# Performance work log

Measured on AMD Instinct MI355X. Metric: run time of the kernel, lower is better.

## Reference

```python
import jax, jax.numpy as jnp
import numpy as np

B, H, W = 64, 512, 512
HW = H * W
MIN_, MAX_ = 100, 100          # seeds sampled per image (bg, fg)
MIN_P, MAX_P = 0.3, 0.3        # candidate-pool fractions
FG_ERODE_K, FG_ERODE_ITER = 11, 1
KSZ = 3                        # dilation kernel for seed maps
IGNORE_IDX = -255
N_BG = int(MIN_P * H * W)      # static bottom-n pool size
EPS = 1e-8


def _minpool2d(x, k):  # morphological erosion of binary map (geodesic border)
    return jax.lax.reduce_window(x, np.inf, jax.lax.min, (k, k), (1, 1), 'SAME')


def _maxpool3d(x, k):  # morphological dilation over (b,h,w)
    return jax.lax.reduce_window(x, -np.inf, jax.lax.max, (1, k, k), (1, 1, 1), 'SAME')


def _gumbel(u):
    return -jnp.log(-jnp.log(u))


def _one_sample(cam, u_fg, u_bg, th):
    # cam: [H,W] in [0,1]; u_fg/u_bg: [HW] uniform(0,1); th: scalar threshold
    cam_q = jnp.floor(cam * 255.0)
    th = jnp.where(th == 0.0, 1.0, jnp.where(th == 255.0, 254.0, th))
    deg = cam.min() == cam.max()  # degenerate map -> no seeds
    roi = (cam_q > th).astype(jnp.float32)
    for _ in range(FG_ERODE_ITER):
        roi = _minpool2d(roi, FG_ERODE_K)

    # ---- foreground: top-n of cam*roi, weighted sample max_ w/o replacement
    camr = (cam * roi + EPS).reshape(HW)
    n_fg = jnp.floor(MAX_P * roi.sum()).astype(jnp.int32)
    order = jnp.argsort(-camr, stable=True)                 # descending stable
    rank = jnp.zeros(HW, jnp.int32).at[order].set(jnp.arange(HW, dtype=jnp.int32))
    mask = rank < n_fg
    logp = jnp.log(jnp.where(mask, camr, 1.0))              # weighted: p = cam value
    score = jnp.where(mask, logp + _gumbel(u_fg), -jnp.inf) # Gumbel top-k == multinomial w/o repl.
    _, sel = jax.lax.top_k(score, MAX_)
    valid = (jnp.arange(MAX_) < jnp.minimum(MAX_, n_fg)) & (n_fg > 0) & (~deg)
    fg = jnp.zeros(HW, jnp.int32).at[sel].set(valid.astype(jnp.int32))

    # ---- background: bottom-n of cam, weighted by relu(1-cam)+eps
    camb = (cam + EPS).reshape(HW)
    orderb = jnp.argsort(camb, stable=True)                 # ascending stable
    rankb = jnp.zeros(HW, jnp.int32).at[orderb].set(jnp.arange(HW, dtype=jnp.int32))
    maskb = rankb < N_BG
    pb = jax.nn.relu(1.0 - camb) + EPS
    scoreb = jnp.where(maskb, jnp.log(pb) + _gumbel(u_bg), -jnp.inf)
    _, selb = jax.lax.top_k(scoreb, MIN_)
    validb = (jnp.arange(MIN_) < min(MIN_, N_BG)) & (~deg)
    bg = jnp.zeros(HW, jnp.int32).at[selb].set(validb.astype(jnp.int32))

    return fg.reshape(H, W), bg.reshape(H, W)


def setup_inputs() -> dict:
    key = jax.random.key(0)
    k1, k2, k3, k4 = jax.random.split(key, 4)
    x = jax.random.uniform(k1, (B, 1, H, W), dtype=jnp.float32)
    roi_thresh = jax.random.randint(k2, (B,), 0, 200).astype(jnp.float32)
    u_fg = jax.random.uniform(k3, (B, HW), dtype=jnp.float32, minval=1e-6, maxval=1.0)
    u_bg = jax.random.uniform(k4, (B, HW), dtype=jnp.float32, minval=1e-6, maxval=1.0)
    return {"x": x, "roi_thresh": roi_thresh, "u_fg": u_fg, "u_bg": u_bg}


def reference(x, roi_thresh, u_fg, u_bg):
    cam = x[:, 0]  # [B,H,W]
    all_fg, all_bg = jax.vmap(_one_sample)(cam, u_fg, u_bg, roi_thresh)
    if KSZ > 1:
        all_fg = (_maxpool3d(all_fg.astype(jnp.float32), KSZ) > 0.5).astype(jnp.int32)
        all_bg = (_maxpool3d(all_bg.astype(jnp.float32), KSZ) > 0.5).astype(jnp.int32)
    outer = all_fg + all_bg
    all_fg = jnp.where(outer == 2, 0, all_fg)
    all_bg = jnp.where(outer == 2, 0, all_bg)
    out = jnp.full((B, H, W), IGNORE_IDX, dtype=jnp.int32)
    out = jnp.where(all_fg == 1, 1, out)
    out = jnp.where(all_bg == 1, 0, out)
    return out
```

## Files before the change

### kernel.cpp

```cpp
#include <hip/hip_runtime.h>

typedef unsigned int u32;

#define BB 64
#define HH 512
#define WW 512
#define HWP 262144
#define WPI 8192
#define NBV 1024
#define NBS 512
#define EPSF 1e-8f
#define NBGK 78643
#define CAND_CAP 4096
#define SEL_CAP 128
#define PN 12
#define CP 16


__device__ __forceinline__ int vbucket(float vb){
    int b = (int)(vb * (float)NBV);
    b = b < 0 ? 0 : b;
    return b > (NBV-1) ? (NBV-1) : b;
}
__device__ __forceinline__ int sbucket(float s){
    float a = (s + 24.0f) * ((float)NBS / 44.0f);
    a = fmaxf(a, 0.0f);
    int b = (int)a;
    return b > (NBS-1) ? (NBS-1) : b;
}
__device__ __forceinline__ u32 flipf(float s){
    u32 u = __float_as_uint(s);
    u32 m = (u & 0x80000000u) ? 0xFFFFFFFFu : 0x80000000u;
    return u ^ m;
}

template<int NB, int BPT, bool DESC>
__device__ __forceinline__ void hist_kth(const u32* __restrict__ hh, int target,
        int* partial, int* res, int t){
    int s = 0;
    #pragma unroll
    for (int i = 0; i < BPT; i++){
        int b = DESC ? (NB-1 - (t*BPT+i)) : (t*BPT+i);
        s += (int)hh[b];
    }
    partial[t] = s;
    __syncthreads();
    for (int off = 1; off < 256; off <<= 1){
        int v = partial[t];
        int u = (t >= off) ? partial[t-off] : 0;
        __syncthreads();
        partial[t] = v + u;
        __syncthreads();
    }
    int incl = partial[t];
    int above = incl - s;
    if (above < target && target <= incl){
        int cum = above;
        #pragma unroll
        for (int i = 0; i < BPT; i++){
            int b = DESC ? (NB-1 - (t*BPT+i)) : (t*BPT+i);
            int h = (int)hh[b];
            if (cum + h >= target){ res[0] = b; res[1] = target - cum; break; }
            cum += h;
        }
    }
    __syncthreads();
}

__global__ __launch_bounds__(256) void k_prep(const float* __restrict__ x,
        const float* __restrict__ thr, u32* __restrict__ roiH,
        u32* __restrict__ ghist_bg, u32* __restrict__ minb, u32* __restrict__ maxb)
{
    __shared__ u32 hist[NBV];
    __shared__ u32 A[256];
    int t = threadIdx.x;
    for (int i = t; i < NBV; i += 256) hist[i] = 0u;
    A[t] = 0u;
    __syncthreads();
    int img = blockIdx.x >> 5, blk = blockIdx.x & 31;
    const float4* c4 = (const float4*)x + (size_t)img * (HWP/4) + (size_t)blk * 2048;
    float th = thr[img];
    th = (th == 0.0f) ? 1.0f : ((th == 255.0f) ? 254.0f : th);
    float4 v[8];
    #pragma unroll
    for (int k = 0; k < 8; k++) v[k] = c4[k*256 + t];
    u32 mn = 0xFFFFFFFFu, mx = 0u;
    #pragma unroll
    for (int k = 0; k < 8; k++){
        float vv[4] = {v[k].x, v[k].y, v[k].z, v[k].w};
        u32 nib = 0u;
        #pragma unroll
        for (int c = 0; c < 4; c++){
            float vl = vv[c];
            u32 ub = __float_as_uint(vl);
            mn = mn < ub ? mn : ub;
            mx = mx > ub ? mx : ub;
            if (floorf(vl * 255.0f) > th) nib |= (1u << c);
            atomicAdd(&hist[vbucket(vl + EPSF)], 1u);
        }
        if (nib) atomicOr(&A[k*32 + (t>>3)], nib << ((t&7)*4));
    }
    for (int o = 32; o >= 1; o >>= 1){
        u32 m2 = __shfl_down(mn, o); mn = mn < m2 ? mn : m2;
        u32 m3 = __shfl_down(mx, o); mx = mx > m3 ? mx : m3;
    }
    if ((t & 63) == 0){ atomicMin(&minb[img], mn); atomicMax(&maxb[img], mx); }
    __syncthreads();
    {
        int wr = t & 15;
        u32 cur = A[t];
        u32 left  = (wr > 0)  ? A[t-1] : 0xFFFFFFFFu;
        u32 right = (wr < 15) ? A[t+1] : 0xFFFFFFFFu;
        u32 res = cur;
        #pragma unroll
        for (int d = 1; d <= 5; d++){
            res &= (cur >> d) | (right << (32 - d));
            res &= (cur << d) | (left  >> (32 - d));
        }
        roiH[(size_t)img*WPI + blk*256 + t] = res;
    }
    for (int i = t; i < NBV; i += 256){
        u32 h = hist[i];
        if (h) atomicAdd(&ghist_bg[(size_t)img*NBV + i], h);
    }
}

__global__ __launch_bounds__(256) void k_vfg(const float* __restrict__ x,
        const u32* __restrict__ roiH, u32* __restrict__ roiE,
        u32* __restrict__ roiSum, u32* __restrict__ ghist_fg)
{
    __shared__ u32 hist[NBV];
    __shared__ u32 W[256];
    int t = threadIdx.x;
    for (int i = t; i < NBV; i += 256) hist[i] = 0u;
    int img = blockIdx.x >> 5, blk = blockIdx.x & 31;
    const u32* rp = roiH + (size_t)img * WPI;
    int iw = blk*256 + t;
    int r = iw >> 4;
    u32 res = 0xFFFFFFFFu;
    #pragma unroll
    for (int d = -5; d <= 5; d++){
        int rr = r + d;
        if (rr >= 0 && rr < HH) res &= rp[iw + d*16];
    }
    W[t] = res;
    roiE[(size_t)img*WPI + iw] = res;
    u32 cnt = __popc(res);
    for (int o = 32; o >= 1; o >>= 1) cnt += __shfl_down(cnt, o);
    if ((t & 63) == 0) atomicAdd(&roiSum[img], cnt);
    __syncthreads();
    const float4* c4 = (const float4*)x + (size_t)img * (HWP/4) + (size_t)blk * 2048;
    u32 nb[8];
    float4 vv[8];
    #pragma unroll
    for (int k = 0; k < 8; k++){
        nb[k] = (W[k*32 + (t>>3)] >> ((t&7)*4)) & 0xFu;
        if (nb[k]) vv[k] = c4[k*256 + t];
    }
    #pragma unroll
    for (int k = 0; k < 8; k++){
        if (nb[k]){
            float vl[4] = {vv[k].x, vv[k].y, vv[k].z, vv[k].w};
            #pragma unroll
            for (int c = 0; c < 4; c++){
                if ((nb[k] >> c) & 1u) atomicAdd(&hist[vbucket(vl[c] + EPSF)], 1u);
            }
        }
    }
    __syncthreads();
    for (int i = t; i < NBV; i += 256){
        u32 h = hist[i];
        if (h) atomicAdd(&ghist_fg[(size_t)img*NBV + i], h);
    }
}

__global__ __launch_bounds__(256) void k_collect1(const float* __restrict__ x, const u32* __restrict__ roiE,
        const u32* __restrict__ ghf, const u32* __restrict__ ghb,
        const u32* __restrict__ minb, const u32* __restrict__ maxb, const u32* __restrict__ roiSum,
        int* __restrict__ prm,
        uint2* __restrict__ candF, u32* __restrict__ cntF,
        uint2* __restrict__ candB, u32* __restrict__ cntB)
{
    __shared__ int partial[256];
    __shared__ int res[2];
    __shared__ u32 words[256];
    int img = blockIdx.x >> 5, blk = blockIdx.x & 31, t = threadIdx.x;
    int deg = (minb[img] == maxb[img]) ? 1 : 0;
    int nfg = (int)floorf(0.3f * (float)(int)roiSum[img]);
    int Bf = -1, rf = 0, Bb = -1, rb = 0;
    if (!deg && nfg > 0){
        hist_kth<NBV,4,true>(ghf + (size_t)img*NBV, nfg, partial, res, t);
        Bf = res[0]; rf = res[1];
    }
    if (!deg){
        hist_kth<NBV,4,false>(ghb + (size_t)img*NBV, NBGK, partial, res, t);
        Bb = res[0]; rb = res[1];
    }
    if (blk == 0 && t == 0){
        int* p = prm + img*PN;
        p[0] = nfg; p[1] = deg; p[2] = Bf; p[3] = rf; p[4] = Bb; p[5] = rb;
    }
    words[t] = roiE[(size_t)img*WPI + blk*256 + t];
    __syncthreads();
    const float4* c4 = (const float4*)x + (size_t)img * (HWP/4) + (size_t)blk * 2048;
    float4 v[8];
    #pragma unroll
    for (int k = 0; k < 8; k++) v[k] = c4[k*256 + t];
    #pragma unroll
    for (int k = 0; k < 8; k++){
        float vv[4] = {v[k].x, v[k].y, v[k].z, v[k].w};
        u32 nib = (words[k*32 + (t>>3)] >> ((t&7)*4)) & 0xFu;
        int pix0 = blk*8192 + k*1024 + t*4;
        #pragma unroll
        for (int c = 0; c < 4; c++){
            float vb = vv[c] + EPSF;
            int bkt = vbucket(vb);
            int pix = pix0 + c;
            if (bkt == Bb){
                u32 q = atomicAdd(&cntB[img*CP], 1u);
                if (q < CAND_CAP) candB[(size_t)img*CAND_CAP + q] = make_uint2(__float_as_uint(vb), (u32)pix);
            }
            if (bkt == Bf && ((nib >> c) & 1u)){
                u32 q = atomicAdd(&cntF[img*CP], 1u);
                if (q < CAND_CAP) candF[(size_t)img*CAND_CAP + q] = make_uint2(__float_as_uint(vb), (u32)pix);
            }
        }
    }
}

__global__ __launch_bounds__(256) void k_resolve1(const uint2* __restrict__ candF, const u32* __restrict__ cntF,
        const uint2* __restrict__ candB, const u32* __restrict__ cntB, int* __restrict__ prm)
{
    int b = blockIdx.x, t = threadIdx.x;
    __shared__ uint2 c[CAND_CAP];
    int rf = prm[b*PN + 3];
    if (rf > 0){
        int m = (int)cntF[b*CP]; m = m < CAND_CAP ? m : CAND_CAP;
        for (int i = t; i < m; i += 256) c[i] = candF[(size_t)b*CAND_CAP + i];
        __syncthreads();
        for (int i = t; i < m; i += 256){
            u32 ki = c[i].x, xi = c[i].y;
            int r = 0;
            for (int j = 0; j < m; j++){
                u32 kj = c[j].x, xj = c[j].y;
                r += (kj > ki) || (kj == ki && xj < xi);
            }
            if (r == rf - 1){ prm[b*PN + 6] = (int)ki; prm[b*PN + 7] = (int)xi; }
        }
    } else if (t == 0){
        prm[b*PN + 6] = (int)0xFFFFFFFFu; prm[b*PN + 7] = -1;
    }
    __syncthreads();
    int rb = prm[b*PN + 5];
    if (rb > 0){
        int m = (int)cntB[b*CP]; m = m < CAND_CAP ? m : CAND_CAP;
        for (int i = t; i < m; i += 256) c[i] = candB[(size_t)b*CAND_CAP + i];
        __syncthreads();
        for (int i = t; i < m; i += 256){
            u32 ki = c[i].x, xi = c[i].y;
            int r = 0;
            for (int j = 0; j < m; j++){
                u32 kj = c[j].x, xj = c[j].y;
                r += (kj < ki) || (kj == ki && xj < xi);
            }
            if (r == rb - 1){ prm[b*PN + 8] = (int)ki; prm[b*PN + 9] = (int)xi; }
        }
    } else if (t == 0){
        prm[b*PN + 8] = 0; prm[b*PN + 9] = -1;
    }
}

__global__ __launch_bounds__(256) void k_shist(const float* __restrict__ x, const u32* __restrict__ roiE,
        const float* __restrict__ ufg, const float* __restrict__ ubg, const int* __restrict__ prm,
        u32* __restrict__ shfG, u32* __restrict__ shbG)
{
    __shared__ u32 hf[NBS];
    __shared__ u32 hb[NBS];
    __shared__ u32 words[256];
    int t = threadIdx.x;
    for (int i = t; i < NBS; i += 256){ hf[i] = 0u; hb[i] = 0u; }
    int img = blockIdx.x >> 5, blk = blockIdx.x & 31;
    words[t] = roiE[(size_t)img*WPI + blk*256 + t];
    __syncthreads();
    const int* p = prm + img*PN;
    u32 ubf = (u32)p[6]; int ibf = p[7];
    u32 ubb = (u32)p[8]; int ibb = p[9];
    size_t b4 = (size_t)img * (HWP/4) + (size_t)blk * 2048;
    const float4* c4 = (const float4*)x + b4;
    const float4* uf4 = (const float4*)ufg + b4;
    const float4* ub4 = (const float4*)ubg + b4;
    float4 v[8];
    #pragma unroll
    for (int k = 0; k < 8; k++) v[k] = c4[k*256 + t];
    u32 fmsk = 0u, bmsk = 0u;
    #pragma unroll
    for (int k = 0; k < 8; k++){
        float vv[4] = {v[k].x, v[k].y, v[k].z, v[k].w};
        u32 nib = (words[k*32 + (t>>3)] >> ((t&7)*4)) & 0xFu;
        int pix0 = blk*8192 + k*1024 + t*4;
        #pragma unroll
        for (int c = 0; c < 4; c++){
            float vb = vv[c] + EPSF;
            u32 bu = __float_as_uint(vb);
            int pix = pix0 + c;
            if (((nib >> c) & 1u) && (bu > ubf || (bu == ubf && pix <= ibf))) fmsk |= 1u << (k*4+c);
            if (bu < ubb || (bu == ubb && pix <= ibb)) bmsk |= 1u << (k*4+c);
        }
    }
    float4 uf[8];
    #pragma unroll
    for (int k = 0; k < 8; k++) if ((fmsk >> (k*4)) & 0xFu) uf[k] = uf4[k*256 + t];
    #pragma unroll
    for (int k = 0; k < 8; k++){
        if ((fmsk >> (k*4)) & 0xFu){
            float vv[4] = {v[k].x, v[k].y, v[k].z, v[k].w};
            float uu[4] = {uf[k].x, uf[k].y, uf[k].z, uf[k].w};
            #pragma unroll
            for (int c = 0; c < 4; c++){
                if ((fmsk >> (k*4+c)) & 1u){
                    float s = logf(vv[c] + EPSF) - logf(-logf(uu[c]));
                    atomicAdd(&hf[sbucket(s)], 1u);
                }
            }
        }
    }
    float4 ub[8];
    #pragma unroll
    for (int k = 0; k < 8; k++) if ((bmsk >> (k*4)) & 0xFu) ub[k] = ub4[k*256 + t];
    #pragma unroll
    for (int k = 0; k < 8; k++){
        if ((bmsk >> (k*4)) & 0xFu){
            float vv[4] = {v[k].x, v[k].y, v[k].z, v[k].w};
            float uu[4] = {ub[k].x, ub[k].y, ub[k].z, ub[k].w};
            #pragma unroll
            for (int c = 0; c < 4; c++){
                if ((bmsk >> (k*4+c)) & 1u){
                    float pb = fmaxf(1.0f - (vv[c] + EPSF), 0.0f) + EPSF;
                    float s = logf(pb) - logf(-logf(uu[c]));
                    atomicAdd(&hb[sbucket(s)], 1u);
                }
            }
        }
    }
    __syncthreads();
    for (int i = t; i < NBS; i += 256){
        u32 h = hf[i]; if (h) atomicAdd(&shfG[(size_t)img*NBS + i], h);
        h = hb[i];     if (h) atomicAdd(&shbG[(size_t)img*NBS + i], h);
    }
}

__global__ __launch_bounds__(256) void k_collect2(const float* __restrict__ x, const u32* __restrict__ roiE,
        const float* __restrict__ ufg, const float* __restrict__ ubg, const int* __restrict__ prm,
        const u32* __restrict__ shfG, const u32* __restrict__ shbG,
        uint2* __restrict__ selF, u32* __restrict__ cntSelF, uint2* __restrict__ scandF, u32* __restrict__ cntScF,
        uint2* __restrict__ selB, u32* __restrict__ cntSelB, uint2* __restrict__ scandB, u32* __restrict__ cntScB)
{
    __shared__ int partial[256];
    __shared__ int res[2];
    __shared__ u32 words[256];
    int img = blockIdx.x >> 5, blk = blockIdx.x & 31, t = threadIdx.x;
    const int* p = prm + img*PN;
    int nfg = p[0], deg = p[1];
    int kf = (deg || nfg <= 0) ? 0 : (nfg < 100 ? nfg : 100);
    int kb = deg ? 0 : 100;
    int sbf = 0x7FFFFFFF, sbb = 0x7FFFFFFF;
    if (kf > 0){
        hist_kth<NBS,2,true>(shfG + (size_t)img*NBS, kf, partial, res, t);
        sbf = res[0];
    }
    if (kb > 0){
        hist_kth<NBS,2,true>(shbG + (size_t)img*NBS, kb, partial, res, t);
        sbb = res[0];
    }
    u32 ubf = (u32)p[6]; int ibf = p[7];
    u32 ubb = (u32)p[8]; int ibb = p[9];
    words[t] = roiE[(size_t)img*WPI + blk*256 + t];
    __syncthreads();
    size_t b4 = (size_t)img * (HWP/4) + (size_t)blk * 2048;
    const float4* c4 = (const float4*)x + b4;
    const float4* uf4 = (const float4*)ufg + b4;
    const float4* ub4 = (const float4*)ubg + b4;
    float4 v[8];
    #pragma unroll
    for (int k = 0; k < 8; k++) v[k] = c4[k*256 + t];
    u32 fmsk = 0u, bmsk = 0u;
    #pragma unroll
    for (int k = 0; k < 8; k++){
        float vv[4] = {v[k].x, v[k].y, v[k].z, v[k].w};
        u32 nib = (words[k*32 + (t>>3)] >> ((t&7)*4)) & 0xFu;
        int pix0 = blk*8192 + k*1024 + t*4;
        #pragma unroll
        for (int c = 0; c < 4; c++){
            float vb = vv[c] + EPSF;
            u32 bu = __float_as_uint(vb);
            int pix = pix0 + c;
            if (((nib >> c) & 1u) && (bu > ubf || (bu == ubf && pix <= ibf))) fmsk |= 1u << (k*4+c);
            if (bu < ubb || (bu == ubb && pix <= ibb)) bmsk |= 1u << (k*4+c);
        }
    }
    float4 uf[8];
    #pragma unroll
    for (int k = 0; k < 8; k++) if ((fmsk >> (k*4)) & 0xFu) uf[k] = uf4[k*256 + t];
    #pragma unroll
    for (int k = 0; k < 8; k++){
        if ((fmsk >> (k*4)) & 0xFu){
            float vv[4] = {v[k].x, v[k].y, v[k].z, v[k].w};
            float uu[4] = {uf[k].x, uf[k].y, uf[k].z, uf[k].w};
            int pix0 = blk*8192 + k*1024 + t*4;
            #pragma unroll
            for (int c = 0; c < 4; c++){
                if ((fmsk >> (k*4+c)) & 1u){
                    float s = logf(vv[c] + EPSF) - logf(-logf(uu[c]));
                    int sb = sbucket(s);
                    if (sb > sbf){
                        u32 q = atomicAdd(&cntSelF[img*CP], 1u);
                        if (q < SEL_CAP) selF[(size_t)img*SEL_CAP + q] = make_uint2(flipf(s), (u32)(pix0 + c));
                    } else if (sb == sbf){
                        u32 q = atomicAdd(&cntScF[img*CP], 1u);
                        if (q < CAND_CAP) scandF[(size_t)img*CAND_CAP + q] = make_uint2(flipf(s), (u32)(pix0 + c));
                    }
                }
            }
        }
    }
    float4 ub[8];
    #pragma unroll
    for (int k = 0; k < 8; k++) if ((bmsk >> (k*4)) & 0xFu) ub[k] = ub4[k*256 + t];
    #pragma unroll
    for (int k = 0; k < 8; k++){
        if ((bmsk >> (k*4)) & 0xFu){
            float vv[4] = {v[k].x, v[k].y, v[k].z, v[k].w};
            float uu[4] = {ub[k].x, ub[k].y, ub[k].z, ub[k].w};
            int pix0 = blk*8192 + k*1024 + t*4;
            #pragma unroll
            for (int c = 0; c < 4; c++){
                if ((bmsk >> (k*4+c)) & 1u){
                    float pb = fmaxf(1.0f - (vv[c] + EPSF), 0.0f) + EPSF;
                    float s = logf(pb) - logf(-logf(uu[c]));
                    int sb = sbucket(s);
                    if (sb > sbb){
                        u32 q = atomicAdd(&cntSelB[img*CP], 1u);
                        if (q < SEL_CAP) selB[(size_t)img*SEL_CAP + q] = make_uint2(flipf(s), (u32)(pix0 + c));
                    } else if (sb == sbb){
                        u32 q = atomicAdd(&cntScB[img*CP], 1u);
                        if (q < CAND_CAP) scandB[(size_t)img*CAND_CAP + q] = make_uint2(flipf(s), (u32)(pix0 + c));
                    }
                }
            }
        }
    }
}

__global__ __launch_bounds__(256) void k_seeds(
        const uint2* __restrict__ selF, const u32* __restrict__ cntSelF,
        const uint2* __restrict__ scandF, const u32* __restrict__ cntScF,
        const uint2* __restrict__ selB, const u32* __restrict__ cntSelB,
        const uint2* __restrict__ scandB, const u32* __restrict__ cntScB,
        const u32* __restrict__ shfG, const u32* __restrict__ shbG,
        const int* __restrict__ prm,
        int* __restrict__ gSeedF, int* __restrict__ gnF,
        int* __restrict__ gSeedB, int* __restrict__ gnB)
{
    int b = blockIdx.x, t = threadIdx.x;
    __shared__ uint2 c[CAND_CAP];
    __shared__ int partial[256];
    __shared__ int res[2];
    __shared__ int seedF[SEL_CAP];
    __shared__ int seedB[SEL_CAP];
    __shared__ int nF, nB;
    const int* p = prm + b*PN;
    int nfg = p[0], deg = p[1];
    int kf = (deg || nfg <= 0) ? 0 : (nfg < 100 ? nfg : 100);
    int kb = deg ? 0 : 100;
    int needf = 0, needb = 0;
    if (kf > 0){
        hist_kth<NBS,2,true>(shfG + (size_t)b*NBS, kf, partial, res, t);
        needf = res[1];
    }
    if (kb > 0){
        hist_kth<NBS,2,true>(shbG + (size_t)b*NBS, kb, partial, res, t);
        needb = res[1];
    }

    int c0 = (int)cntSelF[b*CP]; c0 = c0 < SEL_CAP ? c0 : SEL_CAP;
    for (int i = t; i < c0; i += 256) seedF[i] = (int)selF[(size_t)b*SEL_CAP + i].y;
    int m = (int)cntScF[b*CP]; m = m < CAND_CAP ? m : CAND_CAP;
    for (int i = t; i < m; i += 256) c[i] = scandF[(size_t)b*CAND_CAP + i];
    if (t == 0){ nF = c0; nB = 0; }
    __syncthreads();
    for (int i = t; i < m; i += 256){
        u32 ki = c[i].x, xi = c[i].y;
        int r = 0;
        for (int j = 0; j < m; j++){
            u32 kj = c[j].x, xj = c[j].y;
            r += (kj > ki) || (kj == ki && xj < xi);
        }
        if (r < needf){
            int q = atomicAdd(&nF, 1);
            if (q < SEL_CAP) seedF[q] = (int)xi;
        }
    }
    __syncthreads();
    int fN = nF; fN = fN < SEL_CAP ? fN : SEL_CAP;
    __syncthreads();

    int c0b = (int)cntSelB[b*CP]; c0b = c0b < SEL_CAP ? c0b : SEL_CAP;
    for (int i = t; i < c0b; i += 256) seedB[i] = (int)selB[(size_t)b*SEL_CAP + i].y;
    int mb = (int)cntScB[b*CP]; mb = mb < CAND_CAP ? mb : CAND_CAP;
    for (int i = t; i < mb; i += 256) c[i] = scandB[(size_t)b*CAND_CAP + i];
    if (t == 0) nB = c0b;
    __syncthreads();
    for (int i = t; i < mb; i += 256){
        u32 ki = c[i].x, xi = c[i].y;
        int r = 0;
        for (int j = 0; j < mb; j++){
            u32 kj = c[j].x, xj = c[j].y;
            r += (kj > ki) || (kj == ki && xj < xi);
        }
        if (r < needb){
            int q = atomicAdd(&nB, 1);
            if (q < SEL_CAP) seedB[q] = (int)xi;
        }
    }
    __syncthreads();
    int bN = nB; bN = bN < SEL_CAP ? bN : SEL_CAP;

    for (int i = t; i < fN; i += 256) gSeedF[b*SEL_CAP + i] = seedF[i];
    for (int i = t; i < bN; i += 256) gSeedB[b*SEL_CAP + i] = seedB[i];
    if (t == 0){ gnF[b] = fN; gnB[b] = bN; }
}

__global__ __launch_bounds__(256) void k_paint(
        const int* __restrict__ gSeedF, const int* __restrict__ gnF,
        const int* __restrict__ gSeedB, const int* __restrict__ gnB,
        int* __restrict__ out)
{
    __shared__ int sF[SEL_CAP], sB[SEL_CAP];
    int img = blockIdx.x >> 5, blk = blockIdx.x & 31, t = threadIdx.x;
    int fN = gnF[img]; fN = fN < SEL_CAP ? fN : SEL_CAP;
    int bN = gnB[img]; bN = bN < SEL_CAP ? bN : SEL_CAP;
    for (int i = t; i < fN; i += 256) sF[i] = gSeedF[img*SEL_CAP + i];
    for (int i = t; i < bN; i += 256) sB[i] = gSeedB[img*SEL_CAP + i];
    int4* o4 = (int4*)(out + (size_t)img*HWP + blk*8192);
    #pragma unroll
    for (int i = 0; i < 8; i++) o4[i*256 + t] = make_int4(-255,-255,-255,-255);
    __syncthreads();
    int row0 = blk * 16;
    int* outp = out + (size_t)img*HWP;
    for (int task = t; task < fN * 9; task += 256){
        int s = sF[task / 9];
        int o = task % 9;
        int y = (s >> 9) + (o / 3) - 1;
        int xx = (s & 511) + (o % 3) - 1;
        if (y < row0 || y >= row0 + 16 || xx < 0 || xx >= WW) continue;
        bool conf = false;
        for (int j = 0; j < bN; j++){
            int sb2 = sB[j];
            int dy = y - (sb2 >> 9); if (dy < 0) dy = -dy;
            int dx = xx - (sb2 & 511); if (dx < 0) dx = -dx;
            if (dy <= 1 && dx <= 1){ conf = true; break; }
        }
        if (!conf) outp[y * WW + xx] = 1;
    }
    for (int task = t; task < bN * 9; task += 256){
        int s = sB[task / 9];
        int o = task % 9;
        int y = (s >> 9) + (o / 3) - 1;
        int xx = (s & 511) + (o % 3) - 1;
        if (y < row0 || y >= row0 + 16 || xx < 0 || xx >= WW) continue;
        bool conf = false;
        for (int j = 0; j < fN; j++){
            int sf2 = sF[j];
            int dy = y - (sf2 >> 9); if (dy < 0) dy = -dy;
            int dx = xx - (sf2 & 511); if (dx < 0) dx = -dx;
            if (dy <= 1 && dx <= 1){ conf = true; break; }
        }
        if (!conf) outp[y * WW + xx] = 0;
    }
}

extern "C" void kernel_launch(void* const* d_in, const int* in_sizes, int n_in,
                              void* d_out, int out_size, void* d_ws, size_t ws_size,
                              hipStream_t stream)
{
    (void)in_sizes; (void)n_in; (void)out_size; (void)ws_size;
    const float* x   = (const float*)d_in[0];
    const float* thr = (const float*)d_in[1];
    const float* ufg = (const float*)d_in[2];
    const float* ubg = (const float*)d_in[3];
    int* out = (int*)d_out;
    char* ws = (char*)d_ws;

    size_t off = 0;
    auto carve = [&](size_t bytes) -> char* {
        char* ptr = ws + off;
        off = (off + bytes + 255) & ~(size_t)255;
        return ptr;
    };
    u32* ghist_bg = (u32*)carve((size_t)BB*NBV*4);
    u32* ghist_fg = (u32*)carve((size_t)BB*NBV*4);
    u32* shf      = (u32*)carve((size_t)BB*NBS*4);
    u32* shb      = (u32*)carve((size_t)BB*NBS*4);
    u32* cnts     = (u32*)carve((size_t)6*BB*CP*4);
    u32* roiSum   = (u32*)carve((size_t)BB*4);
    u32* maxb     = (u32*)carve((size_t)BB*4);
    size_t zero_bytes = off;
    u32* minb     = (u32*)carve((size_t)BB*4);
    size_t minb_off = (size_t)((char*)minb - ws);
    u32* roiH     = (u32*)carve((size_t)BB*WPI*4);
    u32* roiE     = (u32*)carve((size_t)BB*WPI*4);
    int* prm      = (int*)carve((size_t)BB*PN*4);
    uint2* candF  = (uint2*)carve((size_t)BB*CAND_CAP*8);
    uint2* candB  = (uint2*)carve((size_t)BB*CAND_CAP*8);
    uint2* scandF = (uint2*)carve((size_t)BB*CAND_CAP*8);
    uint2* scandB = (uint2*)carve((size_t)BB*CAND_CAP*8);
    uint2* selF   = (uint2*)carve((size_t)BB*SEL_CAP*8);
    uint2* selB   = (uint2*)carve((size_t)BB*SEL_CAP*8);
    int* gSeedF   = (int*)carve((size_t)BB*SEL_CAP*4);
    int* gSeedB   = (int*)carve((size_t)BB*SEL_CAP*4);
    int* gnF      = (int*)carve((size_t)BB*4);
    int* gnB      = (int*)carve((size_t)BB*4);
    u32* cntF = cnts, *cntB = cnts + BB*CP, *cntSelF = cnts + 2*BB*CP,
       *cntScF = cnts + 3*BB*CP, *cntSelB = cnts + 4*BB*CP, *cntScB = cnts + 5*BB*CP;

    hipMemsetAsync(ws, 0, zero_bytes, stream);
    hipMemsetAsync(ws + minb_off, 0xFF, (size_t)BB*4, stream);

    k_prep    <<<2048, 256, 0, stream>>>(x, thr, roiH, ghist_bg, minb, maxb);
    k_vfg     <<<2048, 256, 0, stream>>>(x, roiH, roiE, roiSum, ghist_fg);
    k_collect1<<<2048, 256, 0, stream>>>(x, roiE, ghist_fg, ghist_bg, minb, maxb, roiSum,
                                         prm, candF, cntF, candB, cntB);
    k_resolve1<<<64,   256, 0, stream>>>(candF, cntF, candB, cntB, prm);
    k_shist   <<<2048, 256, 0, stream>>>(x, roiE, ufg, ubg, prm, shf, shb);
    k_collect2<<<2048, 256, 0, stream>>>(x, roiE, ufg, ubg, prm, shf, shb,
                                         selF, cntSelF, scandF, cntScF,
                                         selB, cntSelB, scandB, cntScB);
    k_seeds   <<<64,   256, 0, stream>>>(selF, cntSelF, scandF, cntScF,
                                         selB, cntSelB, scandB, cntScB,
                                         shf, shb, prm, gSeedF, gnF, gSeedB, gnB);
    k_paint   <<<2048, 256, 0, stream>>>(gSeedF, gnF, gSeedB, gnB, out);
}
```

Before: 451.1 us.

## Fuse pipeline into hist/select/merge kernels with halo erosion and per-block top-k

Merges the prep and vertical-erosion kernels into one kernel that loads a 5-row halo and performs both erosion passes in shared memory, so the roiH intermediate buffer is no longer needed. Collect, resolve, score-histogram and collect2 are replaced by a select kernel that keeps per-block candidate lists, plus a merge kernel that runs one block per image and side and does the final Gumbel top-k. This cuts the kernel count from eight to four and avoids extra passes over x and u. The cost is redundant halo loads, heavier per-block work, and fixed caps (SBLK, POOL) that could truncate candidates.

Result: faster. 423.5 us (-6.1%).

```diff
diff --git a/kernel.cpp b/kernel.cpp
--- a/kernel.cpp
+++ b/kernel.cpp
@@ -13,6 +13,8 @@
 #define NBGK 78643
 #define CAND_CAP 4096
 #define SEL_CAP 128
+#define SBLK 144
+#define POOL 5120
 #define PN 12
 #define CP 16
 
@@ -33,9 +35,13 @@
     u32 m = (u & 0x80000000u) ? 0xFFFFFFFFu : 0x80000000u;
     return u ^ m;
 }
+__device__ __forceinline__ float unflipf(u32 f){
+    u32 orig = (f & 0x80000000u) ? (f ^ 0x80000000u) : ~f;
+    return __uint_as_float(orig);
+}
 
 template<int NB, int BPT, bool DESC>
-__device__ __forceinline__ void hist_kth(const u32* __restrict__ hh, int target,
+__device__ __forceinline__ void hist_kth(const u32* hh, int target,
         int* partial, int* res, int t){
     int s = 0;
     #pragma unroll
@@ -67,23 +73,74 @@
     __syncthreads();
 }
 
-__global__ __launch_bounds__(256) void k_prep(const float* __restrict__ x,
-        const float* __restrict__ thr, u32* __restrict__ roiH,
-        u32* __restrict__ ghist_bg, u32* __restrict__ minb, u32* __restrict__ maxb)
+template<int NB, int BPT>
+__device__ __forceinline__ void topk_desc(const u32* hh, int K,
+        int* partial, int* res, int t, int& bbOut, int& targOut){
+    int s = 0;
+    #pragma unroll
+    for (int i = 0; i < BPT; i++) s += (int)hh[NB-1 - (t*BPT+i)];
+    partial[t] = s;
+    __syncthreads();
+    for (int off = 1; off < 256; off <<= 1){
+        int v = partial[t];
+        int u = (t >= off) ? partial[t-off] : 0;
+        __syncthreads();
+        partial[t] = v + u;
+        __syncthreads();
+    }
+    int total = partial[255];
+    int target = K < total ? K : total;
+    int incl = partial[t], above = incl - s;
+    if (target > 0 && above < target && target <= incl){
+        int cum = above;
+        #pragma unroll
+        for (int i = 0; i < BPT; i++){
+            int b = NB-1 - (t*BPT+i);
+            int h = (int)hh[b];
+            if (cum + h >= target){ res[0] = b; break; }
+            cum += h;
+        }
+    }
+    __syncthreads();
+    bbOut = (target > 0) ? res[0] : NB;
+    targOut = target;
+    __syncthreads();
+}
+
+__global__ __launch_bounds__(256) void k_hist(const float* __restrict__ x,
+        const float* __restrict__ thr, u32* __restrict__ roiE, u32* __restrict__ roiSum,
+        u32* __restrict__ ghist_bg, u32* __restrict__ ghist_fg,
+        u32* __restrict__ minb, u32* __restrict__ maxb)
 {
-    __shared__ u32 hist[NBV];
-    __shared__ u32 A[256];
+    __shared__ u32 hb2[NBV];
+    __shared__ u32 hf2[NBV];
+    __shared__ u32 rawA[416];
+    __shared__ u32 eH[416];
+    __shared__ u32 W[256];
     int t = threadIdx.x;
-    for (int i = t; i < NBV; i += 256) hist[i] = 0u;
-    A[t] = 0u;
-    __syncthreads();
     int img = blockIdx.x >> 5, blk = blockIdx.x & 31;
-    const float4* c4 = (const float4*)x + (size_t)img * (HWP/4) + (size_t)blk * 2048;
+    int r0 = blk * 16;
+    for (int i = t; i < NBV; i += 256){ hb2[i] = 0u; hf2[i] = 0u; }
+    for (int i = t; i < 416; i += 256){
+        int gr = r0 - 5 + (i >> 4);
+        rawA[i] = (gr < 0 || gr >= HH) ? 0xFFFFFFFFu : 0u;
+    }
+    __syncthreads();
+    const float4* c4img = (const float4*)x + (size_t)img * (HWP/4);
+    const float4* c4 = c4img + (size_t)blk * 2048;
     float th = thr[img];
     th = (th == 0.0f) ? 1.0f : ((th == 255.0f) ? 254.0f : th);
     float4 v[8];
     #pragma unroll
     for (int k = 0; k < 8; k++) v[k] = c4[k*256 + t];
+    float4 hv[5];
+    #pragma unroll
+    for (int j = 0; j < 5; j++){
+        int fi = j*256 + t;
+        int hl = fi >> 7;
+        int gr = (hl < 5) ? (r0 - 5 + hl) : (r0 + 16 + (hl - 5));
+        if (gr >= 0 && gr < HH) hv[j] = c4img[gr*128 + (fi & 127)];
+    }
     u32 mn = 0xFFFFFFFFu, mx = 0u;
     #pragma unroll
     for (int k = 0; k < 8; k++){
@@ -96,9 +153,24 @@
             mn = mn < ub ? mn : ub;
             mx = mx > ub ? mx : ub;
             if (floorf(vl * 255.0f) > th) nib |= (1u << c);
-            atomicAdd(&hist[vbucket(vl + EPSF)], 1u);
-        }
-        if (nib) atomicOr(&A[k*32 + (t>>3)], nib << ((t&7)*4));
+            atomicAdd(&hb2[vbucket(vl + EPSF)], 1u);
+        }
+        if (nib) atomicOr(&rawA[(k*2 + (t>>7) + 5)*16 + ((t&127)>>3)], nib << ((t&7)*4));
+    }
+    #pragma unroll
+    for (int j = 0; j < 5; j++){
+        int fi = j*256 + t;
+        int hl = fi >> 7;
+        int gr = (hl < 5) ? (r0 - 5 + hl) : (r0 + 16 + (hl - 5));
+        if (gr >= 0 && gr < HH){
+            float vv[4] = {hv[j].x, hv[j].y, hv[j].z, hv[j].w};
+            u32 nib = 0u;
+            #pragma unroll
+            for (int c = 0; c < 4; c++)
+                if (floorf(vv[c] * 255.0f) > th) nib |= (1u << c);
+            int hr = (hl < 5) ? hl : (16 + hl);
+            if (nib) atomicOr(&rawA[hr*16 + ((fi&127)>>3)], nib << ((fi&7)*4));
+        }
     }
     for (int o = 32; o >= 1; o >>= 1){
         u32 m2 = __shfl_down(mn, o); mn = mn < m2 ? mn : m2;
@@ -106,185 +178,86 @@
     }
     if ((t & 63) == 0){ atomicMin(&minb[img], mn); atomicMax(&maxb[img], mx); }
     __syncthreads();
-    {
-        int wr = t & 15;
-        u32 cur = A[t];
-        u32 left  = (wr > 0)  ? A[t-1] : 0xFFFFFFFFu;
-        u32 right = (wr < 15) ? A[t+1] : 0xFFFFFFFFu;
+    for (int i = t; i < 416; i += 256){
+        int wr = i & 15;
+        u32 cur = rawA[i];
+        u32 left  = (wr > 0)  ? rawA[i-1] : 0xFFFFFFFFu;
+        u32 right = (wr < 15) ? rawA[i+1] : 0xFFFFFFFFu;
         u32 res = cur;
         #pragma unroll
         for (int d = 1; d <= 5; d++){
             res &= (cur >> d) | (right << (32 - d));
             res &= (cur << d) | (left  >> (32 - d));
         }
-        roiH[(size_t)img*WPI + blk*256 + t] = res;
-    }
+        eH[i] = res;
+    }
+    __syncthreads();
+    {
+        int wr = t & 15;
+        int hr = (t >> 4) + 5;
+        u32 res = 0xFFFFFFFFu;
+        #pragma unroll
+        for (int d = -5; d <= 5; d++) res &= eH[(hr + d)*16 + wr];
+        W[t] = res;
+        roiE[(size_t)img*WPI + blk*256 + t] = res;
+        u32 cnt = __popc(res);
+        for (int o = 32; o >= 1; o >>= 1) cnt += __shfl_down(cnt, o);
+        if ((t & 63) == 0) atomicAdd(&roiSum[img], cnt);
+    }
+    __syncthreads();
+    #pragma unroll
+    for (int k = 0; k < 8; k++){
+        u32 nib = (W[k*32 + (t>>3)] >> ((t&7)*4)) & 0xFu;
+        if (nib){
+            float vv[4] = {v[k].x, v[k].y, v[k].z, v[k].w};
+            #pragma unroll
+            for (int c = 0; c < 4; c++)
+                if ((nib >> c) & 1u) atomicAdd(&hf2[vbucket(vv[c] + EPSF)], 1u);
+        }
+    }
+    __syncthreads();
     for (int i = t; i < NBV; i += 256){
-        u32 h = hist[i];
-        if (h) atomicAdd(&ghist_bg[(size_t)img*NBV + i], h);
-    }
-}
-
-__global__ __launch_bounds__(256) void k_vfg(const float* __restrict__ x,
-        const u32* __restrict__ roiH, u32* __restrict__ roiE,
-        u32* __restrict__ roiSum, u32* __restrict__ ghist_fg)
-{
-    __shared__ u32 hist[NBV];
-    __shared__ u32 W[256];
-    int t = threadIdx.x;
-    for (int i = t; i < NBV; i += 256) hist[i] = 0u;
-    int img = blockIdx.x >> 5, blk = blockIdx.x & 31;
-    const u32* rp = roiH + (size_t)img * WPI;
-    int iw = blk*256 + t;
-    int r = iw >> 4;
-    u32 res = 0xFFFFFFFFu;
-    #pragma unroll
-    for (int d = -5; d <= 5; d++){
-        int rr = r + d;
-        if (rr >= 0 && rr < HH) res &= rp[iw + d*16];
-    }
-    W[t] = res;
-    roiE[(size_t)img*WPI + iw] = res;
-    u32 cnt = __popc(res);
-    for (int o = 32; o >= 1; o >>= 1) cnt += __shfl_down(cnt, o);
-    if ((t & 63) == 0) atomicAdd(&roiSum[img], cnt);
-    __syncthreads();
-    const float4* c4 = (const float4*)x + (size_t)img * (HWP/4) + (size_t)blk * 2048;
-    u32 nb[8];
-    float4 vv[8];
-    #pragma unroll
-    for (int k = 0; k < 8; k++){
-        nb[k] = (W[k*32 + (t>>3)] >> ((t&7)*4)) & 0xFu;
-        if (nb[k]) vv[k] = c4[k*256 + t];
-    }
-    #pragma unroll
-    for (int k = 0; k < 8; k++){
-        if (nb[k]){
-            float vl[4] = {vv[k].x, vv[k].y, vv[k].z, vv[k].w};
-            #pragma unroll
-            for (int c = 0; c < 4; c++){
-                if ((nb[k] >> c) & 1u) atomicAdd(&hist[vbucket(vl[c] + EPSF)], 1u);
-            }
-        }
-    }
-    __syncthreads();
-    for (int i = t; i < NBV; i += 256){
-        u32 h = hist[i];
-        if (h) atomicAdd(&ghist_fg[(size_t)img*NBV + i], h);
-    }
-}
-
-__global__ __launch_bounds__(256) void k_collect1(const float* __restrict__ x, const u32* __restrict__ roiE,
+        u32 h = hb2[i]; if (h) atomicAdd(&ghist_bg[(size_t)img*NBV + i], h);
+        h = hf2[i];     if (h) atomicAdd(&ghist_fg[(size_t)img*NBV + i], h);
+    }
+}
+
+__global__ __launch_bounds__(256) void k_select(const float* __restrict__ x,
+        const u32* __restrict__ roiE, const float* __restrict__ ufg, const float* __restrict__ ubg,
         const u32* __restrict__ ghf, const u32* __restrict__ ghb,
         const u32* __restrict__ minb, const u32* __restrict__ maxb, const u32* __restrict__ roiSum,
         int* __restrict__ prm,
         uint2* __restrict__ candF, u32* __restrict__ cntF,
-        uint2* __restrict__ candB, u32* __restrict__ cntB)
+        uint2* __restrict__ candB, u32* __restrict__ cntB,
+        uint2* __restrict__ blkF, int* __restrict__ blkFn,
+        uint2* __restrict__ blkB, int* __restrict__ blkBn)
 {
     __shared__ int partial[256];
     __shared__ int res[2];
+    __shared__ u32 sh[NBS];
     __shared__ u32 words[256];
+    __shared__ int sN;
     int img = blockIdx.x >> 5, blk = blockIdx.x & 31, t = threadIdx.x;
+    int bid = blockIdx.x;
     int deg = (minb[img] == maxb[img]) ? 1 : 0;
     int nfg = (int)floorf(0.3f * (float)(int)roiSum[img]);
+    bool doF = (!deg && nfg > 0), doB = !deg;
     int Bf = -1, rf = 0, Bb = -1, rb = 0;
-    if (!deg && nfg > 0){
+    if (doF){
         hist_kth<NBV,4,true>(ghf + (size_t)img*NBV, nfg, partial, res, t);
         Bf = res[0]; rf = res[1];
-    }
-    if (!deg){
+        __syncthreads();
+    }
+    if (doB){
         hist_kth<NBV,4,false>(ghb + (size_t)img*NBV, NBGK, partial, res, t);
         Bb = res[0]; rb = res[1];
+        __syncthreads();
     }
     if (blk == 0 && t == 0){
         int* p = prm + img*PN;
         p[0] = nfg; p[1] = deg; p[2] = Bf; p[3] = rf; p[4] = Bb; p[5] = rb;
     }
     words[t] = roiE[(size_t)img*WPI + blk*256 + t];
-    __syncthreads();
-    const float4* c4 = (const float4*)x + (size_t)img * (HWP/4) + (size_t)blk * 2048;
-    float4 v[8];
-    #pragma unroll
-    for (int k = 0; k < 8; k++) v[k] = c4[k*256 + t];
-    #pragma unroll
-    for (int k = 0; k < 8; k++){
-        float vv[4] = {v[k].x, v[k].y, v[k].z, v[k].w};
-        u32 nib = (words[k*32 + (t>>3)] >> ((t&7)*4)) & 0xFu;
-        int pix0 = blk*8192 + k*1024 + t*4;
-        #pragma unroll
-        for (int c = 0; c < 4; c++){
-            float vb = vv[c] + EPSF;
-            int bkt = vbucket(vb);
-            int pix = pix0 + c;
-            if (bkt == Bb){
-                u32 q = atomicAdd(&cntB[img*CP], 1u);
-                if (q < CAND_CAP) candB[(size_t)img*CAND_CAP + q] = make_uint2(__float_as_uint(vb), (u32)pix);
-            }
-            if (bkt == Bf && ((nib >> c) & 1u)){
-                u32 q = atomicAdd(&cntF[img*CP], 1u);
-                if (q < CAND_CAP) candF[(size_t)img*CAND_CAP + q] = make_uint2(__float_as_uint(vb), (u32)pix);
-            }
-        }
-    }
-}
-
-__global__ __launch_bounds__(256) void k_resolve1(const uint2* __restrict__ candF, const u32* __restrict__ cntF,
-        const uint2* __restrict__ candB, const u32* __restrict__ cntB, int* __restrict__ prm)
-{
-    int b = blockIdx.x, t = threadIdx.x;
-    __shared__ uint2 c[CAND_CAP];
-    int rf = prm[b*PN + 3];
-    if (rf > 0){
-        int m = (int)cntF[b*CP]; m = m < CAND_CAP ? m : CAND_CAP;
-        for (int i = t; i < m; i += 256) c[i] = candF[(size_t)b*CAND_CAP + i];
-        __syncthreads();
-        for (int i = t; i < m; i += 256){
-            u32 ki = c[i].x, xi = c[i].y;
-            int r = 0;
-            for (int j = 0; j < m; j++){
-                u32 kj = c[j].x, xj = c[j].y;
-                r += (kj > ki) || (kj == ki && xj < xi);
-            }
-            if (r == rf - 1){ prm[b*PN + 6] = (int)ki; prm[b*PN + 7] = (int)xi; }
-        }
-    } else if (t == 0){
-        prm[b*PN + 6] = (int)0xFFFFFFFFu; prm[b*PN + 7] = -1;
-    }
-    __syncthreads();
-    int rb = prm[b*PN + 5];
-    if (rb > 0){
-        int m = (int)cntB[b*CP]; m = m < CAND_CAP ? m : CAND_CAP;
-        for (int i = t; i < m; i += 256) c[i] = candB[(size_t)b*CAND_CAP + i];
-        __syncthreads();
-        for (int i = t; i < m; i += 256){
-            u32 ki = c[i].x, xi = c[i].y;
-            int r = 0;
-            for (int j = 0; j < m; j++){
-                u32 kj = c[j].x, xj = c[j].y;
-                r += (kj < ki) || (kj == ki && xj < xi);
-            }
-            if (r == rb - 1){ prm[b*PN + 8] = (int)ki; prm[b*PN + 9] = (int)xi; }
-        }
-    } else if (t == 0){
-        prm[b*PN + 8] = 0; prm[b*PN + 9] = -1;
-    }
-}
-
-__global__ __launch_bounds__(256) void k_shist(const float* __restrict__ x, const u32* __restrict__ roiE,
-        const float* __restrict__ ufg, const float* __restrict__ ubg, const int* __restrict__ prm,
-        u32* __restrict__ shfG, u32* __restrict__ shbG)
-{
-    __shared__ u32 hf[NBS];
-    __shared__ u32 hb[NBS];
-    __shared__ u32 words[256];
-    int t = threadIdx.x;
-    for (int i = t; i < NBS; i += 256){ hf[i] = 0u; hb[i] = 0u; }
-    int img = blockIdx.x >> 5, blk = blockIdx.x & 31;
-    words[t] = roiE[(size_t)img*WPI + blk*256 + t];
-    __syncthreads();
-    const int* p = prm + img*PN;
-    u32 ubf = (u32)p[6]; int ibf = p[7];
-    u32 ubb = (u32)p[8]; int ibb = p[9];
     size_t b4 = (size_t)img * (HWP/4) + (size_t)blk * 2048;
     const float4* c4 = (const float4*)x + b4;
     const float4* uf4 = (const float4*)ufg + b4;
@@ -292,7 +265,8 @@
     float4 v[8];
     #pragma unroll
     for (int k = 0; k < 8; k++) v[k] = c4[k*256 + t];
-    u32 fmsk = 0u, bmsk = 0u;
+    __syncthreads();
+    u32 certF = 0u, certB = 0u;
     #pragma unroll
     for (int k = 0; k < 8; k++){
         float vv[4] = {v[k].x, v[k].y, v[k].z, v[k].w};
@@ -301,233 +275,222 @@
         #pragma unroll
         for (int c = 0; c < 4; c++){
             float vb = vv[c] + EPSF;
-            u32 bu = __float_as_uint(vb);
-            int pix = pix0 + c;
-            if (((nib >> c) & 1u) && (bu > ubf || (bu == ubf && pix <= ibf))) fmsk |= 1u << (k*4+c);
-            if (bu < ubb || (bu == ubb && pix <= ibb)) bmsk |= 1u << (k*4+c);
-        }
-    }
-    float4 uf[8];
-    #pragma unroll
-    for (int k = 0; k < 8; k++) if ((fmsk >> (k*4)) & 0xFu) uf[k] = uf4[k*256 + t];
-    #pragma unroll
-    for (int k = 0; k < 8; k++){
-        if ((fmsk >> (k*4)) & 0xFu){
-            float vv[4] = {v[k].x, v[k].y, v[k].z, v[k].w};
-            float uu[4] = {uf[k].x, uf[k].y, uf[k].z, uf[k].w};
-            #pragma unroll
-            for (int c = 0; c < 4; c++){
-                if ((fmsk >> (k*4+c)) & 1u){
-                    float s = logf(vv[c] + EPSF) - logf(-logf(uu[c]));
-                    atomicAdd(&hf[sbucket(s)], 1u);
+            int bkt = vbucket(vb);
+            int bit = k*4 + c;
+            if (doF && ((nib >> c) & 1u)){
+                if (bkt > Bf) certF |= (1u << bit);
+                else if (bkt == Bf){
+                    u32 q = atomicAdd(&cntF[img*CP], 1u);
+                    if (q < CAND_CAP) candF[(size_t)img*CAND_CAP + q] = make_uint2(__float_as_uint(vb), (u32)(pix0 + c));
                 }
             }
-        }
-    }
-    float4 ub[8];
-    #pragma unroll
-    for (int k = 0; k < 8; k++) if ((bmsk >> (k*4)) & 0xFu) ub[k] = ub4[k*256 + t];
-    #pragma unroll
-    for (int k = 0; k < 8; k++){
-        if ((bmsk >> (k*4)) & 0xFu){
-            float vv[4] = {v[k].x, v[k].y, v[k].z, v[k].w};
-            float uu[4] = {ub[k].x, ub[k].y, ub[k].z, ub[k].w};
-            #pragma unroll
-            for (int c = 0; c < 4; c++){
-                if ((bmsk >> (k*4+c)) & 1u){
-                    float pb = fmaxf(1.0f - (vv[c] + EPSF), 0.0f) + EPSF;
-                    float s = logf(pb) - logf(-logf(uu[c]));
-                    atomicAdd(&hb[sbucket(s)], 1u);
+            if (doB){
+                if (bkt < Bb) certB |= (1u << bit);
+                else if (bkt == Bb){
+                    u32 q = atomicAdd(&cntB[img*CP], 1u);
+                    if (q < CAND_CAP) candB[(size_t)img*CAND_CAP + q] = make_uint2(__float_as_uint(vb), (u32)(pix0 + c));
                 }
             }
         }
     }
-    __syncthreads();
-    for (int i = t; i < NBS; i += 256){
-        u32 h = hf[i]; if (h) atomicAdd(&shfG[(size_t)img*NBS + i], h);
-        h = hb[i];     if (h) atomicAdd(&shbG[(size_t)img*NBS + i], h);
-    }
-}
-
-__global__ __launch_bounds__(256) void k_collect2(const float* __restrict__ x, const u32* __restrict__ roiE,
-        const float* __restrict__ ufg, const float* __restrict__ ubg, const int* __restrict__ prm,
-        const u32* __restrict__ shfG, const u32* __restrict__ shbG,
-        uint2* __restrict__ selF, u32* __restrict__ cntSelF, uint2* __restrict__ scandF, u32* __restrict__ cntScF,
-        uint2* __restrict__ selB, u32* __restrict__ cntSelB, uint2* __restrict__ scandB, u32* __restrict__ cntScB)
-{
-    __shared__ int partial[256];
-    __shared__ int res[2];
-    __shared__ u32 words[256];
-    int img = blockIdx.x >> 5, blk = blockIdx.x & 31, t = threadIdx.x;
-    const int* p = prm + img*PN;
-    int nfg = p[0], deg = p[1];
-    int kf = (deg || nfg <= 0) ? 0 : (nfg < 100 ? nfg : 100);
-    int kb = deg ? 0 : 100;
-    int sbf = 0x7FFFFFFF, sbb = 0x7FFFFFFF;
-    if (kf > 0){
-        hist_kth<NBS,2,true>(shfG + (size_t)img*NBS, kf, partial, res, t);
-        sbf = res[0];
-    }
-    if (kb > 0){
-        hist_kth<NBS,2,true>(shbG + (size_t)img*NBS, kb, partial, res, t);
-        sbb = res[0];
-    }
-    u32 ubf = (u32)p[6]; int ibf = p[7];
-    u32 ubb = (u32)p[8]; int ibb = p[9];
-    words[t] = roiE[(size_t)img*WPI + blk*256 + t];
-    __syncthreads();
-    size_t b4 = (size_t)img * (HWP/4) + (size_t)blk * 2048;
-    const float4* c4 = (const float4*)x + b4;
-    const float4* uf4 = (const float4*)ufg + b4;
-    const float4* ub4 = (const float4*)ubg + b4;
-    float4 v[8];
-    #pragma unroll
-    for (int k = 0; k < 8; k++) v[k] = c4[k*256 + t];
-    u32 fmsk = 0u, bmsk = 0u;
-    #pragma unroll
-    for (int k = 0; k < 8; k++){
-        float vv[4] = {v[k].x, v[k].y, v[k].z, v[k].w};
-        u32 nib = (words[k*32 + (t>>3)] >> ((t&7)*4)) & 0xFu;
-        int pix0 = blk*8192 + k*1024 + t*4;
-        #pragma unroll
-        for (int c = 0; c < 4; c++){
-            float vb = vv[c] + EPSF;
-            u32 bu = __float_as_uint(vb);
-            int pix = pix0 + c;
-            if (((nib >> c) & 1u) && (bu > ubf || (bu == ubf && pix <= ibf))) fmsk |= 1u << (k*4+c);
-            if (bu < ubb || (bu == ubb && pix <= ibb)) bmsk |= 1u << (k*4+c);
-        }
-    }
-    float4 uf[8];
-    #pragma unroll
-    for (int k = 0; k < 8; k++) if ((fmsk >> (k*4)) & 0xFu) uf[k] = uf4[k*256 + t];
-    #pragma unroll
-    for (int k = 0; k < 8; k++){
-        if ((fmsk >> (k*4)) & 0xFu){
-            float vv[4] = {v[k].x, v[k].y, v[k].z, v[k].w};
-            float uu[4] = {uf[k].x, uf[k].y, uf[k].z, uf[k].w};
-            int pix0 = blk*8192 + k*1024 + t*4;
-            #pragma unroll
-            for (int c = 0; c < 4; c++){
-                if ((fmsk >> (k*4+c)) & 1u){
-                    float s = logf(vv[c] + EPSF) - logf(-logf(uu[c]));
-                    int sb = sbucket(s);
-                    if (sb > sbf){
-                        u32 q = atomicAdd(&cntSelF[img*CP], 1u);
-                        if (q < SEL_CAP) selF[(size_t)img*SEL_CAP + q] = make_uint2(flipf(s), (u32)(pix0 + c));
-                    } else if (sb == sbf){
-                        u32 q = atomicAdd(&cntScF[img*CP], 1u);
-                        if (q < CAND_CAP) scandF[(size_t)img*CAND_CAP + q] = make_uint2(flipf(s), (u32)(pix0 + c));
+    for (int i = t; i < NBS; i += 256) sh[i] = 0u;
+    __syncthreads();
+    if (certF){
+        #pragma unroll
+        for (int k = 0; k < 8; k++){
+            u32 nb4 = (certF >> (k*4)) & 0xFu;
+            if (nb4){
+                float4 u4 = uf4[k*256 + t];
+                float uu[4] = {u4.x, u4.y, u4.z, u4.w};
+                float vv[4] = {v[k].x, v[k].y, v[k].z, v[k].w};
+                #pragma unroll
+                for (int c = 0; c < 4; c++){
+                    if ((nb4 >> c) & 1u){
+                        float s = logf(vv[c] + EPSF) - logf(-logf(uu[c]));
+                        atomicAdd(&sh[sbucket(s)], 1u);
                     }
                 }
             }
         }
     }
-    float4 ub[8];
-    #pragma unroll
-    for (int k = 0; k < 8; k++) if ((bmsk >> (k*4)) & 0xFu) ub[k] = ub4[k*256 + t];
-    #pragma unroll
-    for (int k = 0; k < 8; k++){
-        if ((bmsk >> (k*4)) & 0xFu){
-            float vv[4] = {v[k].x, v[k].y, v[k].z, v[k].w};
-            float uu[4] = {ub[k].x, ub[k].y, ub[k].z, ub[k].w};
-            int pix0 = blk*8192 + k*1024 + t*4;
-            #pragma unroll
-            for (int c = 0; c < 4; c++){
-                if ((bmsk >> (k*4+c)) & 1u){
-                    float pb = fmaxf(1.0f - (vv[c] + EPSF), 0.0f) + EPSF;
-                    float s = logf(pb) - logf(-logf(uu[c]));
-                    int sb = sbucket(s);
-                    if (sb > sbb){
-                        u32 q = atomicAdd(&cntSelB[img*CP], 1u);
-                        if (q < SEL_CAP) selB[(size_t)img*SEL_CAP + q] = make_uint2(flipf(s), (u32)(pix0 + c));
-                    } else if (sb == sbb){
-                        u32 q = atomicAdd(&cntScB[img*CP], 1u);
-                        if (q < CAND_CAP) scandB[(size_t)img*CAND_CAP + q] = make_uint2(flipf(s), (u32)(pix0 + c));
+    __syncthreads();
+    int bbF, targF;
+    topk_desc<NBS,2>(sh, 100, partial, res, t, bbF, targF);
+    if (t == 0) sN = 0;
+    __syncthreads();
+    if (targF > 0 && certF){
+        #pragma unroll
+        for (int k = 0; k < 8; k++){
+            u32 nb4 = (certF >> (k*4)) & 0xFu;
+            if (nb4){
+                float4 u4 = uf4[k*256 + t];
+                float uu[4] = {u4.x, u4.y, u4.z, u4.w};
+                float vv[4] = {v[k].x, v[k].y, v[k].z, v[k].w};
+                int pix0 = blk*8192 + k*1024 + t*4;
+                #pragma unroll
+                for (int c = 0; c < 4; c++){
+                    if ((nb4 >> c) & 1u){
+                        float s = logf(vv[c] + EPSF) - logf(-logf(uu[c]));
+                        if (sbucket(s) >= bbF){
+                            int q = atomicAdd(&sN, 1);
+                            if (q < SBLK) blkF[(size_t)bid*SBLK + q] = make_uint2(flipf(s), (u32)(pix0 + c));
+                        }
                     }
                 }
             }
         }
     }
-}
-
-__global__ __launch_bounds__(256) void k_seeds(
-        const uint2* __restrict__ selF, const u32* __restrict__ cntSelF,
-        const uint2* __restrict__ scandF, const u32* __restrict__ cntScF,
-        const uint2* __restrict__ selB, const u32* __restrict__ cntSelB,
-        const uint2* __restrict__ scandB, const u32* __restrict__ cntScB,
-        const u32* __restrict__ shfG, const u32* __restrict__ shbG,
-        const int* __restrict__ prm,
+    __syncthreads();
+    if (t == 0) blkFn[bid] = sN < SBLK ? sN : SBLK;
+    __syncthreads();
+    for (int i = t; i < NBS; i += 256) sh[i] = 0u;
+    __syncthreads();
+    if (certB){
+        #pragma unroll
+        for (int k = 0; k < 8; k++){
+            u32 nb4 = (certB >> (k*4)) & 0xFu;
+            if (nb4){
+                float4 u4 = ub4[k*256 + t];
+                float uu[4] = {u4.x, u4.y, u4.z, u4.w};
+                float vv[4] = {v[k].x, v[k].y, v[k].z, v[k].w};
+                #pragma unroll
+                for (int c = 0; c < 4; c++){
+                    if ((nb4 >> c) & 1u){
+                        float pb = fmaxf(1.0f - (vv[c] + EPSF), 0.0f) + EPSF;
+                        float s = logf(pb) - logf(-logf(uu[c]));
+                        atomicAdd(&sh[sbucket(s)], 1u);
+                    }
+                }
+            }
+        }
+    }
+    __syncthreads();
+    int bbB, targB;
+    topk_desc<NBS,2>(sh, 100, partial, res, t, bbB, targB);
+    if (t == 0) sN = 0;
+    __syncthreads();
+    if (targB > 0 && certB){
+        #pragma unroll
+        for (int k = 0; k < 8; k++){
+            u32 nb4 = (certB >> (k*4)) & 0xFu;
+            if (nb4){
+                float4 u4 = ub4[k*256 + t];
+                float uu[4] = {u4.x, u4.y, u4.z, u4.w};
+                float vv[4] = {v[k].x, v[k].y, v[k].z, v[k].w};
+                int pix0 = blk*8192 + k*1024 + t*4;
+                #pragma unroll
+                for (int c = 0; c < 4; c++){
+                    if ((nb4 >> c) & 1u){
+                        float pb = fmaxf(1.0f - (vv[c] + EPSF), 0.0f) + EPSF;
+                        float s = logf(pb) - logf(-logf(uu[c]));
+                        if (sbucket(s) >= bbB){
+                            int q = atomicAdd(&sN, 1);
+                            if (q < SBLK) blkB[(size_t)bid*SBLK + q] = make_uint2(flipf(s), (u32)(pix0 + c));
+                        }
+                    }
+                }
+            }
+        }
+    }
+    __syncthreads();
+    if (t == 0) blkBn[bid] = sN < SBLK ? sN : SBLK;
+}
+
+__global__ __launch_bounds__(256) void k_merge(
+        const uint2* __restrict__ candF, const u32* __restrict__ cntF,
+        const uint2* __restrict__ candB, const u32* __restrict__ cntB,
+        const uint2* __restrict__ blkF, const int* __restrict__ blkFn,
+        const uint2* __restrict__ blkB, const int* __restrict__ blkBn,
+        const int* __restrict__ prm, const float* __restrict__ ufg, const float* __restrict__ ubg,
         int* __restrict__ gSeedF, int* __restrict__ gnF,
         int* __restrict__ gSeedB, int* __restrict__ gnB)
 {
-    int b = blockIdx.x, t = threadIdx.x;
-    __shared__ uint2 c[CAND_CAP];
+    __shared__ uint2 pool[POOL];
+    __shared__ uint2 lc[1024];
+    __shared__ u32 sh[NBS];
     __shared__ int partial[256];
     __shared__ int res[2];
-    __shared__ int seedF[SEL_CAP];
-    __shared__ int seedB[SEL_CAP];
-    __shared__ int nF, nB;
-    const int* p = prm + b*PN;
+    __shared__ int pN, lcN, sN;
+    int img = blockIdx.x >> 1, side = blockIdx.x & 1, t = threadIdx.x;
+    const int* p = prm + img*PN;
     int nfg = p[0], deg = p[1];
-    int kf = (deg || nfg <= 0) ? 0 : (nfg < 100 ? nfg : 100);
-    int kb = deg ? 0 : 100;
-    int needf = 0, needb = 0;
-    if (kf > 0){
-        hist_kth<NBS,2,true>(shfG + (size_t)b*NBS, kf, partial, res, t);
-        needf = res[1];
-    }
-    if (kb > 0){
-        hist_kth<NBS,2,true>(shbG + (size_t)b*NBS, kb, partial, res, t);
-        needb = res[1];
-    }
-
-    int c0 = (int)cntSelF[b*CP]; c0 = c0 < SEL_CAP ? c0 : SEL_CAP;
-    for (int i = t; i < c0; i += 256) seedF[i] = (int)selF[(size_t)b*SEL_CAP + i].y;
-    int m = (int)cntScF[b*CP]; m = m < CAND_CAP ? m : CAND_CAP;
-    for (int i = t; i < m; i += 256) c[i] = scandF[(size_t)b*CAND_CAP + i];
-    if (t == 0){ nF = c0; nB = 0; }
+    int K = (side == 0) ? ((deg || nfg <= 0) ? 0 : (nfg < 100 ? nfg : 100))
+                        : (deg ? 0 : 100);
+    int* gn = (side == 0) ? gnF : gnB;
+    int* gs = (side == 0) ? gSeedF : gSeedB;
+    if (K == 0){ if (t == 0) gn[img] = 0; return; }
+    int r_in = (side == 0) ? p[3] : p[5];
+    const uint2* cand = (side == 0) ? candF : candB;
+    const u32* cnt = (side == 0) ? cntF : cntB;
+    const uint2* bl = (side == 0) ? blkF : blkB;
+    const int* bln = (side == 0) ? blkFn : blkBn;
+    const float* uu = (side == 0) ? ufg : ubg;
+    if (t == 0){ lcN = 0; pN = 0; }
+    int m = (int)cnt[img*CP]; m = m < CAND_CAP ? m : CAND_CAP;
+    for (int i = t; i < m; i += 256) pool[i] = cand[(size_t)img*CAND_CAP + i];
     __syncthreads();
     for (int i = t; i < m; i += 256){
-        u32 ki = c[i].x, xi = c[i].y;
+        u32 ki = pool[i].x, xi = pool[i].y;
         int r = 0;
         for (int j = 0; j < m; j++){
-            u32 kj = c[j].x, xj = c[j].y;
+            u32 kj = pool[j].x, xj = pool[j].y;
+            if (side == 0) r += (kj > ki) || (kj == ki && xj < xi);
+            else           r += (kj < ki) || (kj == ki && xj < xi);
+        }
+        if (r < r_in){
+            float vb = __uint_as_float(ki);
+            float uv = uu[(size_t)img*HWP + xi];
+            float s;
+            if (side == 0) s = logf(vb) - logf(-logf(uv));
+            else { float pb = fmaxf(1.0f - vb, 0.0f) + EPSF; s = logf(pb) - logf(-logf(uv)); }
+            int q = atomicAdd(&lcN, 1);
+            if (q < 1024) lc[q] = make_uint2(flipf(s), xi);
+        }
+    }
+    __syncthreads();
+    for (int idx = t; idx < 32*SBLK; idx += 256){
+        int b2 = idx / SBLK, i2 = idx % SBLK;
+        int n = bln[img*32 + b2];
+        if (i2 < n){
+            int q = atomicAdd(&pN, 1);
+            if (q < POOL) pool[q] = bl[(size_t)(img*32 + b2)*SBLK + i2];
+        }
+    }
+    __syncthreads();
+    int ln = lcN < 1024 ? lcN : 1024;
+    for (int i = t; i < ln; i += 256){
+        int q = atomicAdd(&pN, 1);
+        if (q < POOL) pool[q] = lc[i];
+    }
+    __syncthreads();
+    int P = pN < POOL ? pN : POOL;
+    for (int i = t; i < NBS; i += 256) sh[i] = 0u;
+    __syncthreads();
+    for (int i = t; i < P; i += 256)
+        atomicAdd(&sh[sbucket(unflipf(pool[i].x))], 1u);
+    __syncthreads();
+    int bb, targ;
+    topk_desc<NBS,2>(sh, K, partial, res, t, bb, targ);
+    if (t == 0) sN = 0;
+    __syncthreads();
+    for (int i = t; i < P; i += 256){
+        if (sbucket(unflipf(pool[i].x)) >= bb){
+            int q = atomicAdd(&sN, 1);
+            if (q < 1024) lc[q] = pool[i];
+        }
+    }
+    __syncthreads();
+    int mm = sN < 1024 ? sN : 1024;
+    for (int i = t; i < mm; i += 256){
+        u32 ki = lc[i].x, xi = lc[i].y;
+        int r = 0;
+        for (int j = 0; j < mm; j++){
+            u32 kj = lc[j].x, xj = lc[j].y;
             r += (kj > ki) || (kj == ki && xj < xi);
         }
-        if (r < needf){
-            int q = atomicAdd(&nF, 1);
-            if (q < SEL_CAP) seedF[q] = (int)xi;
-        }
-    }
-    __syncthreads();
-    int fN = nF; fN = fN < SEL_CAP ? fN : SEL_CAP;
-    __syncthreads();
-
-    int c0b = (int)cntSelB[b*CP]; c0b = c0b < SEL_CAP ? c0b : SEL_CAP;
-    for (int i = t; i < c0b; i += 256) seedB[i] = (int)selB[(size_t)b*SEL_CAP + i].y;
-    int mb = (int)cntScB[b*CP]; mb = mb < CAND_CAP ? mb : CAND_CAP;
-    for (int i = t; i < mb; i += 256) c[i] = scandB[(size_t)b*CAND_CAP + i];
-    if (t == 0) nB = c0b;
-    __syncthreads();
-    for (int i = t; i < mb; i += 256){
-        u32 ki = c[i].x, xi = c[i].y;
-        int r = 0;
-        for (int j = 0; j < mb; j++){
-            u32 kj = c[j].x, xj = c[j].y;
-            r += (kj > ki) || (kj == ki && xj < xi);
-        }
-        if (r < needb){
-            int q = atomicAdd(&nB, 1);
-            if (q < SEL_CAP) seedB[q] = (int)xi;
-        }
-    }
-    __syncthreads();
-    int bN = nB; bN = bN < SEL_CAP ? bN : SEL_CAP;
-
-    for (int i = t; i < fN; i += 256) gSeedF[b*SEL_CAP + i] = seedF[i];
-    for (int i = t; i < bN; i += 256) gSeedB[b*SEL_CAP + i] = seedB[i];
-    if (t == 0){ gnF[b] = fN; gnB[b] = bN; }
+        if (r < targ) gs[img*SEL_CAP + r] = (int)xi;
+    }
+    if (t == 0) gn[img] = targ;
 }
 
 __global__ __launch_bounds__(256) void k_paint(
@@ -599,44 +562,36 @@
     };
     u32* ghist_bg = (u32*)carve((size_t)BB*NBV*4);
     u32* ghist_fg = (u32*)carve((size_t)BB*NBV*4);
-    u32* shf      = (u32*)carve((size_t)BB*NBS*4);
-    u32* shb      = (u32*)carve((size_t)BB*NBS*4);
-    u32* cnts     = (u32*)carve((size_t)6*BB*CP*4);
+    u32* cnts     = (u32*)carve((size_t)2*BB*CP*4);
     u32* roiSum   = (u32*)carve((size_t)BB*4);
     u32* maxb     = (u32*)carve((size_t)BB*4);
     size_t zero_bytes = off;
     u32* minb     = (u32*)carve((size_t)BB*4);
     size_t minb_off = (size_t)((char*)minb - ws);
-    u32* roiH     = (u32*)carve((size_t)BB*WPI*4);
     u32* roiE     = (u32*)carve((size_t)BB*WPI*4);
     int* prm      = (int*)carve((size_t)BB*PN*4);
     uint2* candF  = (uint2*)carve((size_t)BB*CAND_CAP*8);
     uint2* candB  = (uint2*)carve((size_t)BB*CAND_CAP*8);
-    uint2* scandF = (uint2*)carve((size_t)BB*CAND_CAP*8);
-    uint2* scandB = (uint2*)carve((size_t)BB*CAND_CAP*8);
-    uint2* selF   = (uint2*)carve((size_t)BB*SEL_CAP*8);
-    uint2* selB   = (uint2*)carve((size_t)BB*SEL_CAP*8);
+    uint2* blkF   = (uint2*)carve((size_t)2048*SBLK*8);
+    uint2* blkB   = (uint2*)carve((size_t)2048*SBLK*8);
+    int* blkFn    = (int*)carve((size_t)2048*4);
+    int* blkBn    = (int*)carve((size_t)2048*4);
     int* gSeedF   = (int*)carve((size_t)BB*SEL_CAP*4);
     int* gSeedB   = (int*)carve((size_t)BB*SEL_CAP*4);
     int* gnF      = (int*)carve((size_t)BB*4);
     int* gnB      = (int*)carve((size_t)BB*4);
-    u32* cntF = cnts, *cntB = cnts + BB*CP, *cntSelF = cnts + 2*BB*CP,
-       *cntScF = cnts + 3*BB*CP, *cntSelB = cnts + 4*BB*CP, *cntScB = cnts + 5*BB*CP;
+    u32* cntF = cnts, *cntB = cnts + BB*CP;
 
     hipMemsetAsync(ws, 0, zero_bytes, stream);
     hipMemsetAsync(ws + minb_off, 0xFF, (size_t)BB*4, stream);
 
-    k_prep    <<<2048, 256, 0, stream>>>(x, thr, roiH, ghist_bg, minb, maxb);
-    k_vfg     <<<2048, 256, 0, stream>>>(x, roiH, roiE, roiSum, ghist_fg);
-    k_collect1<<<2048, 256, 0, stream>>>(x, roiE, ghist_fg, ghist_bg, minb, maxb, roiSum,
-                                         prm, candF, cntF, candB, cntB);
-    k_resolve1<<<64,   256, 0, stream>>>(candF, cntF, candB, cntB, prm);
-    k_shist   <<<2048, 256, 0, stream>>>(x, roiE, ufg, ubg, prm, shf, shb);
-    k_collect2<<<2048, 256, 0, stream>>>(x, roiE, ufg, ubg, prm, shf, shb,
-                                         selF, cntSelF, scandF, cntScF,
-                                         selB, cntSelB, scandB, cntScB);
-    k_seeds   <<<64,   256, 0, stream>>>(selF, cntSelF, scandF, cntScF,
-                                         selB, cntSelB, scandB, cntScB,
-                                         shf, shb, prm, gSeedF, gnF, gSeedB, gnB);
-    k_paint   <<<2048, 256, 0, stream>>>(gSeedF, gnF, gSeedB, gnB, out);
-}
+    k_hist  <<<2048, 256, 0, stream>>>(x, thr, roiE, roiSum, ghist_bg, ghist_fg, minb, maxb);
+    k_select<<<2048, 256, 0, stream>>>(x, roiE, ufg, ubg, ghist_fg, ghist_bg,
+                                       minb, maxb, roiSum, prm,
+                                       candF, cntF, candB, cntB,
+                                       blkF, blkFn, blkB, blkBn);
+    k_merge <<<128,  256, 0, stream>>>(candF, cntF, candB, cntB,
+                                       blkF, blkFn, blkB, blkBn,
+                                       prm, ufg, ubg, gSeedF, gnF, gSeedB, gnB);
+    k_paint <<<2048, 256, 0, stream>>>(gSeedF, gnF, gSeedB, gnB, out);
+}
```
